# Kernel optimization log

Measured on AMD Instinct MI355X. Metric: run time of the kernel, lower is better.

## Reference

```python
import jax, jax.numpy as jnp
import numpy as np

B, L, D_MODEL, H, D_K, D_V, C = 4, 2048, 512, 8, 64, 64, 5
LN_EPS = 1e-5


def setup_inputs() -> dict:
    key = jax.random.key(0)
    ks = jax.random.split(key, 9)
    u_k = min(int(C * np.log(L)), L)  # 38
    s = 1.0 / np.sqrt(D_MODEL)
    return {
        "input_Q": jax.random.normal(ks[0], (B, L, D_MODEL), jnp.float32),
        "input_K": jax.random.normal(ks[1], (B, L, D_MODEL), jnp.float32),
        "input_V": jax.random.normal(ks[2], (B, L, D_MODEL), jnp.float32),
        "W_Q": jax.random.normal(ks[3], (D_MODEL, H * D_K), jnp.float32) * s,
        "W_K": jax.random.normal(ks[4], (D_MODEL, H * D_K), jnp.float32) * s,
        "W_V": jax.random.normal(ks[5], (D_MODEL, H * D_V), jnp.float32) * s,
        "W_fc": jax.random.normal(ks[6], (H * D_V, D_MODEL), jnp.float32) * (1.0 / np.sqrt(H * D_V)),
        "ln_gamma": jnp.ones((D_MODEL,), jnp.float32),
        "ln_beta": jnp.zeros((D_MODEL,), jnp.float32),
        "index_sample": jax.random.randint(ks[7], (L, u_k), 0, L, jnp.int32),
    }


def reference(input_Q, input_K, input_V, W_Q, W_K, W_V, W_fc, ln_gamma, ln_beta, index_sample):
    Bb, L_Q, _ = input_Q.shape
    L_K = input_K.shape[1]
    u_q = min(int(C * np.log(L_Q)), L_Q)  # n_top queries kept

    # projections -> (B, H, L, d)
    Q = (input_Q @ W_Q).reshape(Bb, L_Q, H, D_K).transpose(0, 2, 1, 3)
    K = (input_K @ W_K).reshape(Bb, L_K, H, D_K).transpose(0, 2, 1, 3)
    V = (input_V @ W_V).reshape(Bb, L_K, H, D_V).transpose(0, 2, 1, 3)

    # sampled QK scores: gather u_k random keys per query position
    K_sample = K[:, :, index_sample, :]                      # (B,H,L_Q,u_k,d_k)
    QK_sample = jnp.einsum('bhqe,bhqke->bhqk', Q, K_sample)  # (B,H,L_Q,u_k)

    # sparsity measure M = max - mean, top-u_q queries
    M = QK_sample.max(axis=-1) - QK_sample.mean(axis=-1)     # (B,H,L_Q)
    _, idx = jax.lax.top_k(M, u_q)                           # (B,H,u_q)

    # attention only for selected queries
    Q_sel = jnp.take_along_axis(Q, idx[..., None], axis=2)   # (B,H,u_q,d_k)
    scores = jnp.einsum('bhue,bhke->bhuk', Q_sel, K) / np.sqrt(D_K)
    attn = jax.nn.softmax(scores, axis=-1)
    values = jnp.einsum('bhuk,bhkd->bhud', attn, V)          # (B,H,u_q,d_v)

    # initial context = mean of V (attn_mask is None), scatter selected rows
    context = jnp.broadcast_to(V.mean(axis=2, keepdims=True), (Bb, H, L_Q, D_V))
    bb = jnp.arange(Bb)[:, None, None]
    hh = jnp.arange(H)[None, :, None]
    context = context.at[bb, hh, idx].set(values)

    context = context.transpose(0, 2, 1, 3).reshape(Bb, L_Q, H * D_V)
    out = context @ W_fc                                     # dropout p=0.0

    y = out + input_Q
    mu = y.mean(axis=-1, keepdims=True)
    var = jnp.mean(jnp.square(y - mu), axis=-1, keepdims=True)
    y = (y - mu) / jnp.sqrt(var + LN_EPS) * ln_gamma + ln_beta
    return y, idx
```

## Files before the change

kernel.cpp:

```cpp
#include <hip/hip_runtime.h>
#include <hip/hip_bf16.h>

#define NB 4
#define NL 2048
#define NH 8
#define NDM 512
#define ND 64
#define KSPLIT 4
#define QB 8

__global__ void samp_flag_init(int* __restrict__ flag) {
  if (threadIdx.x == 0 && blockIdx.x == 0) *flag = 0;
}
__global__ void samp_probe(const int* __restrict__ sampAsInt, int* __restrict__ flag, int nwords) {
  const int g = blockIdx.x * 256 + threadIdx.x;
  if (g < nwords) {
    unsigned v = (unsigned)sampAsInt[g];
    if (v >= 2048u) atomicOr(flag, 1);
  }
}
__global__ void samp_convert(const void* __restrict__ samp, const int* __restrict__ flag,
                             int* __restrict__ sampI, int n) {
  const int g = blockIdx.x * 256 + threadIdx.x;
  if (g >= n) return;
  int v;
  if (*flag == 0) v = ((const int*)samp)[g];
  else            v = (int)(((const float*)samp)[g]);
  if (v < 0) v = 0;
  if (v > NL - 1) v = NL - 1;
  sampI[g] = v;
}

__global__ __launch_bounds__(256, 4) void proj3(
    const float* __restrict__ AQ, const float* __restrict__ AK, const float* __restrict__ AV,
    const float* __restrict__ wQm, const float* __restrict__ wKm, const float* __restrict__ wVm,
    int gh0, float* __restrict__ Qc, float* __restrict__ Kc, float* __restrict__ Vc) {
  __shared__ float As_[32 * 132];
  __shared__ float Ws_[32 * 68];
  const int tid = threadIdx.x;
  const int bm = blockIdx.x;
  const int hl = blockIdx.y;
  const int mat = blockIdx.z;
  const int bh = gh0 + hl;
  const int b = bh >> 3, h = bh & 7;
  const float* A = (mat == 0) ? AQ : (mat == 1) ? AK : AV;
  const float* W = (mat == 0) ? wQm : (mat == 1) ? wKm : wVm;
  float* D = (mat == 0) ? Qc : (mat == 1) ? Kc : Vc;
  const float* Ab = A + (size_t)b * NL * NDM;
  const int colbase = h * 64;
  const int tm = tid >> 4, tn = tid & 15;
  float acc[8][4] = {};
  for (int k0 = 0; k0 < 512; k0 += 32) {
#pragma unroll
    for (int i = 0; i < 4; ++i) {
      int s = tid + i * 256;
      int r = s >> 3, c4 = (s & 7) * 4;
      float4 v = *reinterpret_cast<const float4*>(Ab + (size_t)(bm * 128 + r) * 512 + k0 + c4);
      As_[(c4 + 0) * 132 + r] = v.x;
      As_[(c4 + 1) * 132 + r] = v.y;
      As_[(c4 + 2) * 132 + r] = v.z;
      As_[(c4 + 3) * 132 + r] = v.w;
    }
#pragma unroll
    for (int i = 0; i < 2; ++i) {
      int s = tid + i * 256;
      int r = s >> 4, c4 = (s & 15) * 4;
      *reinterpret_cast<float4*>(&Ws_[r * 68 + c4]) =
          *reinterpret_cast<const float4*>(W + (size_t)(k0 + r) * 512 + colbase + c4);
    }
    __syncthreads();
#pragma unroll
    for (int kk = 0; kk < 32; ++kk) {
      float4 a0 = *reinterpret_cast<const float4*>(&As_[kk * 132 + tm * 4]);
      float4 a1 = *reinterpret_cast<const float4*>(&As_[kk * 132 + 64 + tm * 4]);
      float4 w  = *reinterpret_cast<const float4*>(&Ws_[kk * 68 + tn * 4]);
      float a[8] = {a0.x, a0.y, a0.z, a0.w, a1.x, a1.y, a1.z, a1.w};
      float wv[4] = {w.x, w.y, w.z, w.w};
#pragma unroll
      for (int ii = 0; ii < 8; ++ii)
#pragma unroll
        for (int jj = 0; jj < 4; ++jj) acc[ii][jj] += a[ii] * wv[jj];
    }
    __syncthreads();
  }
#pragma unroll
  for (int ii = 0; ii < 8; ++ii) {
    int row = bm * 128 + ((ii < 4) ? (tm * 4 + ii) : (64 + tm * 4 + (ii - 4)));
    float4 v = make_float4(acc[ii][0], acc[ii][1], acc[ii][2], acc[ii][3]);
    *reinterpret_cast<float4*>(D + ((size_t)hl * NL + row) * ND + tn * 4) = v;
  }
}

template <int UK>
__global__ __launch_bounds__(256) void sample_scores_t(
    const float* __restrict__ Q, const float* __restrict__ K,
    const int* __restrict__ sampI, float* __restrict__ M) {
  __shared__ float KsAll[4][UK * 66];
  __shared__ float QsAll[4][68];
  const int wv = threadIdx.x >> 6, l = threadIdx.x & 63;
  const int gq = blockIdx.x * 4 + wv;
  const int hl = gq >> 11;
  const int q = gq & 2047;
  float* Ks = KsAll[wv];
  float* Qs = QsAll[wv];
  const float* Kb = K + (size_t)hl * NL * ND;
  Qs[l] = Q[(size_t)gq * ND + l];
  const int base = __builtin_amdgcn_readfirstlane(q) * UK;
#pragma unroll
  for (int r = 0; r < UK; ++r) {
    int kk = sampI[base + r] & (NL - 1);
    Ks[r * 66 + l] = Kb[(size_t)kk * ND + l];
  }
  __syncthreads();
  const int myk = (l < UK) ? l : (UK - 1);
  float acc = 0.f;
#pragma unroll
  for (int j = 0; j < 32; ++j) {
    float2 kv = *reinterpret_cast<const float2*>(&Ks[myk * 66 + 2 * j]);
    float2 qv = *reinterpret_cast<const float2*>(&Qs[2 * j]);
    acc += kv.x * qv.x + kv.y * qv.y;
  }
  float mval = (l < UK) ? acc : -1e30f;
  float sval = (l < UK) ? acc : 0.f;
#pragma unroll
  for (int o = 32; o; o >>= 1) {
    mval = fmaxf(mval, __shfl_xor(mval, o, 64));
    sval += __shfl_xor(sval, o, 64);
  }
  if (l == 0) M[gq] = mval - sval * (1.f / (float)UK);
}

__global__ void sample_scores_gen(const float* __restrict__ Q, const float* __restrict__ K,
                                  const int* __restrict__ sampI, float* __restrict__ M, int uk) {
  const int wave = threadIdx.x >> 6, lane = threadIdx.x & 63;
  const int gq = blockIdx.x * 4 + wave;
  const int hl = gq >> 11;
  const int q = gq & 2047;
  const float qv = Q[(size_t)gq * ND + lane];
  const float* Kbase = K + (size_t)hl * NL * ND;
  float mx = -1e30f, sm = 0.f;
  for (int k = 0; k < uk; ++k) {
    int kidx = sampI[q * uk + k] & (NL - 1);
    float p = qv * Kbase[(size_t)kidx * ND + lane];
#pragma unroll
    for (int o = 32; o; o >>= 1) p += __shfl_xor(p, o, 64);
    mx = fmaxf(mx, p);
    sm += p;
  }
  if (lane == 0) M[gq] = mx - sm / (float)uk;
}

__global__ void topk_kernel(const float* __restrict__ M, int* __restrict__ idxo,
                            float* __restrict__ outIdx, int uq) {
  __shared__ float mv[2048];
  __shared__ float bwv[4];
  __shared__ int bwi[4];
  const int bh = blockIdx.x, t = threadIdx.x;
  for (int i = 0; i < 8; ++i) mv[t + i * 256] = M[(size_t)bh * 2048 + t + i * 256];
  __syncthreads();
  for (int it = 0; it < uq; ++it) {
    float best = -1e38f; int bidx = 1 << 30;
#pragma unroll
    for (int i = 0; i < 8; ++i) {
      int id = t + i * 256;
      float v = mv[id];
      if (v > best || (v == best && id < bidx)) { best = v; bidx = id; }
    }
#pragma unroll
    for (int o = 32; o; o >>= 1) {
      float ov = __shfl_xor(best, o, 64);
      int oi = __shfl_xor(bidx, o, 64);
      if (ov > best || (ov == best && oi < bidx)) { best = ov; bidx = oi; }
    }
    if ((t & 63) == 0) { bwv[t >> 6] = best; bwi[t >> 6] = bidx; }
    __syncthreads();
    if (t == 0) {
      float bb = bwv[0]; int bi2 = bwi[0];
#pragma unroll
      for (int w = 1; w < 4; ++w) {
        if (bwv[w] > bb || (bwv[w] == bb && bwi[w] < bi2)) { bb = bwv[w]; bi2 = bwi[w]; }
      }
      int sel = bi2 & (NL - 1);
      idxo[bh * uq + it] = sel;
      outIdx[bh * uq + it] = (float)sel;
      mv[sel] = -1e38f;
    }
    __syncthreads();
  }
}

__global__ void vmean_part(const float* __restrict__ V, float* __restrict__ Vmp) {
  __shared__ float red[256];
  const int hl = blockIdx.x, seg = blockIdx.y;
  const int t = threadIdx.x, d = t & 63, sl = t >> 6;
  const float* Vb = V + (size_t)hl * NL * ND;
  float s = 0.f;
  for (int k = seg * 256 + sl; k < seg * 256 + 256; k += 4) s += Vb[(size_t)k * ND + d];
  red[t] = s;
  __syncthreads();
  if (sl == 0)
    Vmp[((size_t)hl * 8 + seg) * ND + d] = red[d] + red[64 + d] + red[128 + d] + red[192 + d];
}
__global__ void vmean_final(const float* __restrict__ Vmp, float* __restrict__ Vmg) {
  const int hl = blockIdx.x, d = threadIdx.x;
  float s = 0.f;
#pragma unroll
  for (int seg = 0; seg < 8; ++seg) s += Vmp[((size_t)hl * 8 + seg) * ND + d];
  Vmg[hl * ND + d] = s * (1.f / 2048.f);
}

__global__ __launch_bounds__(256) void attn_part(
    const float* __restrict__ Qw, const float* __restrict__ Kw, const float* __restrict__ Vw,
    const int* __restrict__ idxo, float* __restrict__ pacc, float* __restrict__ pml, int uq) {
  __shared__ float Qs[QB][68];
  __shared__ float Ks[64][68];
  __shared__ float Vs[64][68];
  __shared__ float sc[QB][66];
  __shared__ float accs[QB][68];
  const int hl = blockIdx.x, qg = blockIdx.y, ks = blockIdx.z;
  const int t = threadIdx.x;
#pragma unroll
  for (int i = 0; i < 2; ++i) {
    int s = t + i * 256;
    int q = s >> 6, d = s & 63;
    int u = qg * QB + q;
    float v = 0.f;
    if (u < uq) {
      int qi = idxo[hl * uq + u] & (NL - 1);
      v = Qw[((size_t)hl * NL + qi) * ND + d];
    }
    Qs[q][d] = v;
    accs[q][d] = 0.f;
  }
  float m_run = -1e30f, l_run = 0.f;
  const int q2 = t >> 5, ln = t & 31;
  __syncthreads();
  const int kbeg = ks * (NL / KSPLIT);
  for (int k0 = kbeg; k0 < kbeg + NL / KSPLIT; k0 += 64) {
#pragma unroll
    for (int i = 0; i < 4; ++i) {
      int s = t + i * 256;
      int r = s >> 4, c4 = (s & 15) * 4;
      *reinterpret_cast<float4*>(&Ks[r][c4]) =
          *reinterpret_cast<const float4*>(Kw + ((size_t)hl * NL + k0 + r) * ND + c4);
      *reinterpret_cast<float4*>(&Vs[r][c4]) =
          *reinterpret_cast<const float4*>(Vw + ((size_t)hl * NL + k0 + r) * ND + c4);
    }
    __syncthreads();
    {
      const int q = t & 7, kk = t >> 3;
      float d0 = 0.f, d1 = 0.f;
#pragma unroll
      for (int dd = 0; dd < 64; dd += 4) {
        float4 qv = *reinterpret_cast<const float4*>(&Qs[q][dd]);
        float4 ka = *reinterpret_cast<const float4*>(&Ks[kk][dd]);
        float4 kb = *reinterpret_cast<const float4*>(&Ks[kk + 32][dd]);
        d0 += qv.x * ka.x + qv.y * ka.y + qv.z * ka.z + qv.w * ka.w;
        d1 += qv.x * kb.x + qv.y * kb.y + qv.z * kb.z + qv.w * kb.w;
      }
      sc[q][kk] = d0 * 0.125f;
      sc[q][kk + 32] = d1 * 0.125f;
    }
    __syncthreads();
    {
      float s0 = sc[q2][ln], s1 = sc[q2][ln + 32];
      float tmax = fmaxf(s0, s1);
#pragma unroll
      for (int o = 16; o; o >>= 1) tmax = fmaxf(tmax, __shfl_xor(tmax, o, 64));
      float mnew = fmaxf(m_run, tmax);
      float scl = __expf(m_run - mnew);
      float p0 = __expf(s0 - mnew), p1 = __expf(s1 - mnew);
      float tsum = p0 + p1;
#pragma unroll
      for (int o = 16; o; o >>= 1) tsum += __shfl_xor(tsum, o, 64);
      l_run = l_run * scl + tsum;
      m_run = mnew;
      sc[q2][ln] = p0; sc[q2][ln + 32] = p1;
      float a0 = accs[q2][2 * ln] * scl, a1 = accs[q2][2 * ln + 1] * scl;
#pragma unroll 8
      for (int k = 0; k < 64; ++k) {
        float p = sc[q2][k];
        a0 += p * Vs[k][2 * ln];
        a1 += p * Vs[k][2 * ln + 1];
      }
      accs[q2][2 * ln] = a0; accs[q2][2 * ln + 1] = a1;
    }
    __syncthreads();
  }
  const int u = qg * QB + q2;
  if (u < uq) {
    size_t g = ((size_t)hl * uq + u) * KSPLIT + ks;
    pacc[g * ND + 2 * ln] = accs[q2][2 * ln];
    pacc[g * ND + 2 * ln + 1] = accs[q2][2 * ln + 1];
    if (ln == 0) { pml[g * 2] = m_run; pml[g * 2 + 1] = l_run; }
  }
}

__global__ void attn_merge(const float* __restrict__ pacc, const float* __restrict__ pml,
                           float* __restrict__ vals, int uq) {
  const int g = blockIdx.x;
  const int d = threadIdx.x;
  float mstar = -1e30f;
#pragma unroll
  for (int s = 0; s < KSPLIT; ++s) mstar = fmaxf(mstar, pml[((size_t)g * KSPLIT + s) * 2]);
  float num = 0.f, den = 0.f;
#pragma unroll
  for (int s = 0; s < KSPLIT; ++s) {
    float e = __expf(pml[((size_t)g * KSPLIT + s) * 2] - mstar);
    den += e * pml[((size_t)g * KSPLIT + s) * 2 + 1];
    num += e * pacc[((size_t)g * KSPLIT + s) * ND + d];
  }
  vals[(size_t)g * ND + d] = num / den;
}

__global__ void selmap_init(short* __restrict__ selmap) {
  const int g = blockIdx.x * 256 + threadIdx.x;
  selmap[g] = -1;
  selmap[g + 32768] = -1;
}
__global__ void selmap_fill(const int* __restrict__ idxo, short* __restrict__ selmap, int uq) {
  const int g = blockIdx.x * 256 + threadIdx.x;
  if (g >= NB * NH * uq) return;
  const int bh = g / uq, u = g - bh * uq;
  const int b = bh >> 3, h = bh & 7;
  const int l = idxo[g] & (NL - 1);
  selmap[((size_t)b * NL + l) * NH + h] = (short)u;
}

__global__ void base_gemm(const float* __restrict__ Vm, const float* __restrict__ Wfc,
                          float* __restrict__ base) {
  __shared__ float vm[512];
  const int b = blockIdx.x, t = threadIdx.x;
  vm[t] = Vm[b * 512 + t];
  vm[t + 256] = Vm[b * 512 + t + 256];
  __syncthreads();
  const int c0 = blockIdx.y * 256 + t;
  float acc = 0.f;
  for (int k = 0; k < 512; ++k) acc += vm[k] * Wfc[(size_t)k * 512 + c0];
  base[b * 512 + c0] = acc;
}

__global__ void corr_gemm(const float* __restrict__ vals, const float* __restrict__ Vm,
                          const float* __restrict__ Wfc, float* __restrict__ corr, int uq) {
  __shared__ float diff[64];
  const int g = blockIdx.x, t = threadIdx.x;
  const int bh = g / uq;
  const int h = bh & 7;
  if (t < 64) diff[t] = vals[(size_t)g * 64 + t] - Vm[bh * 64 + t];
  __syncthreads();
  float a0 = 0.f, a1 = 0.f;
#pragma unroll
  for (int d = 0; d < 64; ++d) {
    a0 += diff[d] * Wfc[(size_t)(h * 64 + d) * 512 + t];
    a1 += diff[d] * Wfc[(size_t)(h * 64 + d) * 512 + t + 256];
  }
  corr[(size_t)g * 512 + t] = a0;
  corr[(size_t)g * 512 + t + 256] = a1;
}

__global__ void ln_fused(const float* __restrict__ base, const float* __restrict__ resid,
                         const float* __restrict__ corr, const short* __restrict__ selmap,
                         const float* __restrict__ gamma, const float* __restrict__ beta,
                         float* __restrict__ out, int uq) {
  __shared__ float red[256];
  const int row = blockIdx.x, t = threadIdx.x;
  const int b = row >> 11;
  float y0 = base[b * 512 + t] + resid[(size_t)row * 512 + t];
  float y1 = base[b * 512 + 256 + t] + resid[(size_t)row * 512 + 256 + t];
#pragma unroll
  for (int h = 0; h < NH; ++h) {
    int s = selmap[(size_t)row * NH + h];
    if (s >= 0 && s < uq) {
      const float* cp = corr + (size_t)((b * NH + h) * uq + s) * 512;
      y0 += cp[t];
      y1 += cp[t + 256];
    }
  }
  red[t] = y0 + y1;
  __syncthreads();
  for (int s = 128; s; s >>= 1) { if (t < s) red[t] += red[t + s]; __syncthreads(); }
  const float mu = red[0] * (1.f / 512.f);
  __syncthreads();
  const float d0 = y0 - mu, d1 = y1 - mu;
  red[t] = d0 * d0 + d1 * d1;
  __syncthreads();
  for (int s = 128; s; s >>= 1) { if (t < s) red[t] += red[t + s]; __syncthreads(); }
  const float rs = rsqrtf(red[0] * (1.f / 512.f) + 1e-5f);
  __syncthreads();
  out[(size_t)row * 512 + t] = d0 * rs * gamma[t] + beta[t];
  out[(size_t)row * 512 + 256 + t] = d1 * rs * gamma[256 + t] + beta[256 + t];
}

extern "C" void kernel_launch(void* const* d_in, const int* in_sizes, int n_in,
                              void* d_out, int out_size, void* d_ws, size_t ws_size,
                              hipStream_t stream) {
  const float* inQ = (const float*)d_in[0];
  const float* inK = (const float*)d_in[1];
  const float* inV = (const float*)d_in[2];
  const float* wQ = (const float*)d_in[3];
  const float* wK = (const float*)d_in[4];
  const float* wV = (const float*)d_in[5];
  const float* wFC = (const float*)d_in[6];
  const float* gamma = (const float*)d_in[7];
  const float* beta = (const float*)d_in[8];
  const void* samp = d_in[9];

  const int nsamp = in_sizes[9];
  const int uk = nsamp / NL;
  const int uq = uk;
  const int nqg = (uq + QB - 1) / QB;

  if (out_size < NB * NL * NDM + NB * NH * uq) return;

  const size_t perH = 3 * 131072 + 2048 + (size_t)uq * KSPLIT * 64 + (size_t)uq * KSPLIT * 2 + 8 * 64;
  const size_t fixed = (size_t)32 * uq * 64 + 2048 + 2048 + (size_t)32 * uq * 512
                     + (size_t)32 * uq + 32768 + (size_t)nsamp + 128;
  int hcg = 0;
  for (int c = 32; c >= 1; c >>= 1) {
    if ((perH * (size_t)c + fixed + 256) * 4ull <= ws_size) { hcg = c; break; }
  }
  if (hcg == 0) return;

  float* ws = (float*)d_ws;
  float* Qc = ws;
  float* Kc = Qc + (size_t)hcg * 131072;
  float* Vc = Kc + (size_t)hcg * 131072;
  float* Mb = Vc + (size_t)hcg * 131072;
  float* pacc = Mb + (size_t)hcg * 2048;
  float* pml = pacc + (size_t)hcg * uq * KSPLIT * 64;
  float* Vmp = pml + (size_t)hcg * uq * KSPLIT * 2;
  float* vals = Vmp + (size_t)hcg * 8 * 64;
  float* Vm = vals + (size_t)32 * uq * 64;
  float* base = Vm + 2048;
  float* corr = base + 2048;
  int* idxo = (int*)(corr + (size_t)32 * uq * 512);
  short* selmap = (short*)(idxo + (size_t)32 * uq);
  int* sampI = (int*)(selmap + 65536);
  int* flag = sampI + nsamp;

  float* out = (float*)d_out;
  float* outIdx = out + (size_t)NB * NL * NDM;

  const int nwords = nsamp / 2;
  samp_flag_init<<<1, 64, 0, stream>>>(flag);
  samp_probe<<<(nwords + 255) / 256, 256, 0, stream>>>((const int*)samp, flag, nwords);
  samp_convert<<<(nsamp + 255) / 256, 256, 0, stream>>>(samp, flag, sampI, nsamp);

  for (int gh0 = 0; gh0 < NB * NH; gh0 += hcg) {
    proj3<<<dim3(16, hcg, 3), 256, 0, stream>>>(inQ, inK, inV, wQ, wK, wV, gh0, Qc, Kc, Vc);
    if (uk == 38)
      sample_scores_t<38><<<hcg * NL / 4, 256, 0, stream>>>(Qc, Kc, sampI, Mb);
    else
      sample_scores_gen<<<hcg * NL / 4, 256, 0, stream>>>(Qc, Kc, sampI, Mb, uk);
    topk_kernel<<<hcg, 256, 0, stream>>>(Mb, idxo + (size_t)gh0 * uq,
                                         outIdx + (size_t)gh0 * uq, uq);
    vmean_part<<<dim3(hcg, 8), 256, 0, stream>>>(Vc, Vmp);
    vmean_final<<<hcg, 64, 0, stream>>>(Vmp, Vm + (size_t)gh0 * ND);
    attn_part<<<dim3(hcg, nqg, KSPLIT), 256, 0, stream>>>(Qc, Kc, Vc,
                                                          idxo + (size_t)gh0 * uq,
                                                          pacc, pml, uq);
    attn_merge<<<hcg * uq, 64, 0, stream>>>(pacc, pml, vals + (size_t)gh0 * uq * ND, uq);
  }

  selmap_init<<<NB * NL * NH / 2 / 256, 256, 0, stream>>>(selmap);
  selmap_fill<<<(NB * NH * uq + 255) / 256, 256, 0, stream>>>(idxo, selmap, uq);
  base_gemm<<<dim3(NB, 2), 256, 0, stream>>>(Vm, wFC, base);
  corr_gemm<<<NB * NH * uq, 256, 0, stream>>>(vals, Vm, wFC, corr, uq);
  ln_fused<<<NB * NL, 256, 0, stream>>>(base, inQ, corr, selmap, gamma, beta, out, uq);
}
```

Baseline: 373.6 us.

## Compute V projection with bf16 MFMA instead of FP32 SIMT GEMM

```diff
diff --git a/kernel.cpp b/kernel.cpp
--- a/kernel.cpp
+++ b/kernel.cpp
@@ -8,6 +8,9 @@
 #define ND 64
 #define KSPLIT 4
 #define QB 8
+
+typedef __attribute__((ext_vector_type(8))) short short8b;
+typedef __attribute__((ext_vector_type(4))) float f32x4;
 
 __global__ void samp_flag_init(int* __restrict__ flag) {
   if (threadIdx.x == 0 && blockIdx.x == 0) *flag = 0;
@@ -31,10 +34,17 @@
   sampI[g] = v;
 }
 
+__global__ void wconv(const float* __restrict__ W, unsigned short* __restrict__ WT) {
+  const int g = blockIdx.x * 256 + threadIdx.x;
+  const int k = g >> 9, c = g & 511;
+  __hip_bfloat16 hb = __float2bfloat16(W[(size_t)k * 512 + c]);
+  WT[(size_t)c * 512 + k] = *reinterpret_cast<unsigned short*>(&hb);
+}
+
 __global__ __launch_bounds__(256, 4) void proj3(
-    const float* __restrict__ AQ, const float* __restrict__ AK, const float* __restrict__ AV,
-    const float* __restrict__ wQm, const float* __restrict__ wKm, const float* __restrict__ wVm,
-    int gh0, float* __restrict__ Qc, float* __restrict__ Kc, float* __restrict__ Vc) {
+    const float* __restrict__ AQ, const float* __restrict__ AK,
+    const float* __restrict__ wQm, const float* __restrict__ wKm,
+    int gh0, float* __restrict__ Qc, float* __restrict__ Kc) {
   __shared__ float As_[32 * 132];
   __shared__ float Ws_[32 * 68];
   const int tid = threadIdx.x;
@@ -43,9 +53,9 @@
   const int mat = blockIdx.z;
   const int bh = gh0 + hl;
   const int b = bh >> 3, h = bh & 7;
-  const float* A = (mat == 0) ? AQ : (mat == 1) ? AK : AV;
-  const float* W = (mat == 0) ? wQm : (mat == 1) ? wKm : wVm;
-  float* D = (mat == 0) ? Qc : (mat == 1) ? Kc : Vc;
+  const float* A = (mat == 0) ? AQ : AK;
+  const float* W = (mat == 0) ? wQm : wKm;
+  float* D = (mat == 0) ? Qc : Kc;
   const float* Ab = A + (size_t)b * NL * NDM;
   const int colbase = h * 64;
   const int tm = tid >> 4, tn = tid & 15;
@@ -88,6 +98,48 @@
     int row = bm * 128 + ((ii < 4) ? (tm * 4 + ii) : (64 + tm * 4 + (ii - 4)));
     float4 v = make_float4(acc[ii][0], acc[ii][1], acc[ii][2], acc[ii][3]);
     *reinterpret_cast<float4*>(D + ((size_t)hl * NL + row) * ND + tn * 4) = v;
+  }
+}
+
+__global__ __launch_bounds__(256) void projV_mfma(
+    const float* __restrict__ AV, const unsigned short* __restrict__ WT,
+    int gh0, float* __restrict__ Vc) {
+  const int wv = threadIdx.x >> 6, l = threadIdx.x & 63;
+  const int bm = blockIdx.x;
+  const int hl = blockIdx.y;
+  const int bh = gh0 + hl;
+  const int b = bh >> 3, h = bh & 7;
+  const float* Ab = AV + (size_t)b * NL * NDM;
+  const int row = bm * 64 + wv * 16 + (l & 15);
+  const int kg = (l >> 4) * 8;
+  f32x4 acc0 = {}, acc1 = {}, acc2 = {}, acc3 = {};
+  for (int k0 = 0; k0 < 512; k0 += 32) {
+    const float* ap = Ab + (size_t)row * 512 + k0 + kg;
+    short8b af;
+#pragma unroll
+    for (int j = 0; j < 8; ++j) {
+      __hip_bfloat16 hb = __float2bfloat16(ap[j]);
+      af[j] = *reinterpret_cast<short*>(&hb);
+    }
+    const unsigned short* wp = WT + (size_t)(h * 64 + (l & 15)) * 512 + k0 + kg;
+    short8b b0 = *reinterpret_cast<const short8b*>(wp);
+    short8b b1 = *reinterpret_cast<const short8b*>(wp + 16 * 512);
+    short8b b2 = *reinterpret_cast<const short8b*>(wp + 32 * 512);
+    short8b b3 = *reinterpret_cast<const short8b*>(wp + 48 * 512);
+    acc0 = __builtin_amdgcn_mfma_f32_16x16x32_bf16(af, b0, acc0, 0, 0, 0);
+    acc1 = __builtin_amdgcn_mfma_f32_16x16x32_bf16(af, b1, acc1, 0, 0, 0);
+    acc2 = __builtin_amdgcn_mfma_f32_16x16x32_bf16(af, b2, acc2, 0, 0, 0);
+    acc3 = __builtin_amdgcn_mfma_f32_16x16x32_bf16(af, b3, acc3, 0, 0, 0);
+  }
+  const int rbase = bm * 64 + wv * 16 + (l >> 4) * 4;
+  const int col = l & 15;
+#pragma unroll
+  for (int j = 0; j < 4; ++j) {
+    size_t o = ((size_t)hl * NL + rbase + j) * ND + col;
+    Vc[o] = acc0[j];
+    Vc[o + 16] = acc1[j];
+    Vc[o + 32] = acc2[j];
+    Vc[o + 48] = acc3[j];
   }
 }
 
@@ -414,7 +466,7 @@
 
   const size_t perH = 3 * 131072 + 2048 + (size_t)uq * KSPLIT * 64 + (size_t)uq * KSPLIT * 2 + 8 * 64;
   const size_t fixed = (size_t)32 * uq * 64 + 2048 + 2048 + (size_t)32 * uq * 512
-                     + (size_t)32 * uq + 32768 + (size_t)nsamp + 128;
+                     + (size_t)32 * uq + 32768 + (size_t)nsamp + 131072 + 256;
   int hcg = 0;
   for (int c = 32; c >= 1; c >>= 1) {
     if ((perH * (size_t)c + fixed + 256) * 4ull <= ws_size) { hcg = c; break; }
@@ -437,6 +489,7 @@
   short* selmap = (short*)(idxo + (size_t)32 * uq);
   int* sampI = (int*)(selmap + 65536);
   int* flag = sampI + nsamp;
+  unsigned short* WTv = (unsigned short*)(flag + 64);
 
   float* out = (float*)d_out;
   float* outIdx = out + (size_t)NB * NL * NDM;
@@ -445,9 +498,11 @@
   samp_flag_init<<<1, 64, 0, stream>>>(flag);
   samp_probe<<<(nwords + 255) / 256, 256, 0, stream>>>((const int*)samp, flag, nwords);
   samp_convert<<<(nsamp + 255) / 256, 256, 0, stream>>>(samp, flag, sampI, nsamp);
+  wconv<<<1024, 256, 0, stream>>>(wV, WTv);
 
   for (int gh0 = 0; gh0 < NB * NH; gh0 += hcg) {
-    proj3<<<dim3(16, hcg, 3), 256, 0, stream>>>(inQ, inK, inV, wQ, wK, wV, gh0, Qc, Kc, Vc);
+    proj3<<<dim3(16, hcg, 2), 256, 0, stream>>>(inQ, inK, wQ, wK, gh0, Qc, Kc);
+    projV_mfma<<<dim3(32, hcg), 256, 0, stream>>>(inV, WTv, gh0, Vc);
     if (uk == 38)
       sample_scores_t<38><<<hcg * NL / 4, 256, 0, stream>>>(Qc, Kc, sampI, Mb);
     else
```

After: 370.9 us. About the same (-0.7%).
